# Kernel optimization log

Hardware: AMD Instinct MI355X
Metric: run time of the kernel (lower is better)

The kernel has to match this reference:

```python
import jax, jax.numpy as jnp
import numpy as np

B, K, D = 4096, 16, 256
NUM_CODES = 512
BETA = 0.25  # commitment (activation_entropy=None path)
LN_EPS = 1e-5

def setup_inputs() -> dict:
    key = jax.random.key(0)
    ks = jax.random.split(key, 6)
    hidden = jax.random.normal(ks[0], (B, K, D), dtype=jnp.float32)
    active_mask = jax.random.randint(ks[1], (B, K), 0, 2).astype(bool)
    bound = 1.0 / NUM_CODES
    codebook = jax.random.uniform(ks[2], (NUM_CODES, D), minval=-bound, maxval=bound, dtype=jnp.float32)
    lim = 1.0 / np.sqrt(D)
    W_in = jax.random.uniform(ks[3], (D, D), minval=-lim, maxval=lim, dtype=jnp.float32)
    W_out = jax.random.uniform(ks[4], (D, D), minval=-lim, maxval=lim, dtype=jnp.float32)
    ln_gamma = jnp.ones((D,), jnp.float32)
    ln_beta = jnp.zeros((D,), jnp.float32)
    return {"hidden": hidden, "active_mask": active_mask, "codebook": codebook,
            "W_in": W_in, "W_out": W_out, "ln_gamma": ln_gamma, "ln_beta": ln_beta}

def reference(hidden, active_mask, codebook, W_in, W_out, ln_gamma, ln_beta):
    sg = jax.lax.stop_gradient
    z = jnp.einsum('bkd,ed->bke', hidden, W_in)              # proj_in (no bias)
    z_flat = z.reshape(-1, D)                                 # [B*K, D]
    # ||z - c||^2 = |z|^2 - 2 z.c + |c|^2
    dist = (jnp.sum(z_flat * z_flat, -1, keepdims=True)
            - 2.0 * z_flat @ codebook.T
            + jnp.sum(codebook * codebook, -1))               # [B*K, C]
    idx = jnp.argmin(dist, axis=-1)                           # [B*K]
    z_q = codebook[idx].reshape(z.shape)                      # gather
    vq_loss = jnp.mean((sg(z_q) - z) ** 2) + BETA * jnp.mean((z_q - sg(z)) ** 2)
    z_st = z + sg(z_q - z)                                    # straight-through
    out = jnp.einsum('bkd,ed->bke', z_st, W_out)              # proj_out
    h = hidden + active_mask[..., None].astype(jnp.float32) * out
    mu = jnp.mean(h, -1, keepdims=True)
    var = jnp.mean((h - mu) ** 2, -1, keepdims=True)
    h_comm = (h - mu) * jax.lax.rsqrt(var + LN_EPS) * ln_gamma + ln_beta
    return h_comm, vq_loss
```

## Files before the change

kernel.cpp:

```cpp
#include <hip/hip_runtime.h>

#define LN_EPS 1e-5f

typedef short bf16x8 __attribute__((ext_vector_type(8)));
typedef float f32x4  __attribute__((ext_vector_type(4)));

__device__ __forceinline__ unsigned short f2bf(float f) {
  unsigned u = __float_as_uint(f);
  u += 0x7fffu + ((u >> 16) & 1u);
  return (unsigned short)(u >> 16);
}
__device__ __forceinline__ float bf2f(unsigned short s) {
  return __uint_as_float(((unsigned)s) << 16);
}

__device__ __forceinline__ bf16x8 pack8(float4 a, float4 b) {
  bf16x8 v;
  v[0] = (short)f2bf(a.x); v[1] = (short)f2bf(a.y);
  v[2] = (short)f2bf(a.z); v[3] = (short)f2bf(a.w);
  v[4] = (short)f2bf(b.x); v[5] = (short)f2bf(b.y);
  v[6] = (short)f2bf(b.z); v[7] = (short)f2bf(b.w);
  return v;
}

__global__ __launch_bounds__(256) void prep_kernel(
    const float* __restrict__ codebook, const float* __restrict__ W_in,
    const float* __restrict__ W_out,
    float* __restrict__ loss_acc, unsigned* __restrict__ ticket,
    float* __restrict__ c2, float* __restrict__ code_out,
    unsigned short* __restrict__ BT) {
  const int b = blockIdx.x, t = threadIdx.x;
  __shared__ float As[32][260];
  __shared__ float Bs[16][260];
  __shared__ float Res[32][17];

  if (b < 64) {
    if (b == 0 && t == 0) { *loss_acc = 0.f; *ticket = 0u; }
    int code = b * 8 + (t >> 5);
    const float* src = codebook + (size_t)code * 256 + (t & 31) * 8;
    float4 x0 = *(const float4*)src, x1 = *(const float4*)(src + 4);
    float s = x0.x * x0.x + x0.y * x0.y + x0.z * x0.z + x0.w * x0.w +
              x1.x * x1.x + x1.y * x1.y + x1.z * x1.z + x1.w * x1.w;
    s += __shfl_xor(s, 1);  s += __shfl_xor(s, 2);
    s += __shfl_xor(s, 4);  s += __shfl_xor(s, 8);
    s += __shfl_xor(s, 16);
    if ((t & 31) == 0) c2[code] = s;
    return;
  }

  if (b < 320) {
    int bi = b - 64, ci = bi & 15, ei = bi >> 4;
    {
      int row = t >> 4, col = (t & 15) * 16;
      const float4* s = (const float4*)(W_out + (size_t)(ei * 16 + row) * 256 + col);
      float4* d = (float4*)&Bs[row][col];
      d[0] = s[0]; d[1] = s[1]; d[2] = s[2]; d[3] = s[3];
    }
    {
      int row = t >> 3, col = (t & 7) * 32;
      const float4* s = (const float4*)(codebook + (size_t)(ci * 32 + row) * 256 + col);
      float4* d = (float4*)&As[row][col];
      #pragma unroll
      for (int k = 0; k < 8; k++) d[k] = s[k];
    }
    __syncthreads();
    int c = t & 31, e0 = t >> 5;
    float a0 = 0.f, a1 = 0.f;
    #pragma unroll 4
    for (int d = 0; d < 256; d += 4) {
      float4 cv = *(const float4*)&As[c][d];
      float4 w0 = *(const float4*)&Bs[e0][d];
      float4 w1 = *(const float4*)&Bs[e0 + 8][d];
      a0 += cv.x * w0.x + cv.y * w0.y + cv.z * w0.z + cv.w * w0.w;
      a1 += cv.x * w1.x + cv.y * w1.y + cv.z * w1.z + cv.w * w1.w;
    }
    code_out[(size_t)(ci * 32 + c) * 256 + ei * 16 + e0]     = a0;
    code_out[(size_t)(ci * 32 + c) * 256 + ei * 16 + e0 + 8] = a1;
    return;
  }

  if (b < 576) {
    int bi = b - 320, ci = bi & 15, di = bi >> 4;
    int c0 = ci * 32, d0 = di * 16;
    {
      int e = t;
      const float* src = W_in + (size_t)e * 256 + d0;
      #pragma unroll
      for (int k = 0; k < 4; k++) {
        float4 v = *(const float4*)(src + k * 4);
        Bs[k * 4 + 0][e] = v.x; Bs[k * 4 + 1][e] = v.y;
        Bs[k * 4 + 2][e] = v.z; Bs[k * 4 + 3][e] = v.w;
      }
    }
    {
      int row = t >> 3, col = (t & 7) * 32;
      const float4* s = (const float4*)(codebook + (size_t)(c0 + row) * 256 + col);
      float4* d = (float4*)&As[row][col];
      #pragma unroll
      for (int k = 0; k < 8; k++) d[k] = s[k];
    }
    __syncthreads();
    int c = t & 31, dl = t >> 5;
    float a0 = 0.f, a1 = 0.f;
    #pragma unroll 4
    for (int d = 0; d < 256; d += 4) {
      float4 cv = *(const float4*)&As[c][d];
      float4 w0 = *(const float4*)&Bs[dl][d];
      float4 w1 = *(const float4*)&Bs[dl + 8][d];
      a0 += cv.x * w0.x + cv.y * w0.y + cv.z * w0.z + cv.w * w0.w;
      a1 += cv.x * w1.x + cv.y * w1.y + cv.z * w1.z + cv.w * w1.w;
    }
    Res[c][dl] = a0; Res[c][dl + 8] = a1;
    __syncthreads();
    if (t < 64) {
      int c2i = t & 31, kqo = t >> 5;
      int code = c0 + c2i, dg = d0 + kqo * 8;
      int cl = code & 255;
      int chunk = (code >> 8) * 8 + (dg >> 5);
      int kq = (dg >> 3) & 3;
      float4 x0, x1;
      x0.x = Res[c2i][kqo * 8 + 0]; x0.y = Res[c2i][kqo * 8 + 1];
      x0.z = Res[c2i][kqo * 8 + 2]; x0.w = Res[c2i][kqo * 8 + 3];
      x1.x = Res[c2i][kqo * 8 + 4]; x1.y = Res[c2i][kqo * 8 + 5];
      x1.z = Res[c2i][kqo * 8 + 6]; x1.w = Res[c2i][kqo * 8 + 7];
      *(bf16x8*)(BT + chunk * 8192 + (cl >> 4) * 512 + kq * 128 + (cl & 15) * 8) =
          pack8(x0, x1);
    }
    return;
  }

  {
    int bi = b - 576;
    int ks = bi & 7, bt = bi >> 3;
    int a0c = ks * 32, b0c = bt * 16;
    {
      int e = t;
      const float* srca = W_in + (size_t)e * 256 + a0c;
      #pragma unroll
      for (int k = 0; k < 8; k++) {
        float4 v = *(const float4*)(srca + k * 4);
        As[k * 4 + 0][e] = v.x; As[k * 4 + 1][e] = v.y;
        As[k * 4 + 2][e] = v.z; As[k * 4 + 3][e] = v.w;
      }
      const float* srcb = W_in + (size_t)e * 256 + b0c;
      #pragma unroll
      for (int k = 0; k < 4; k++) {
        float4 v = *(const float4*)(srcb + k * 4);
        Bs[k * 4 + 0][e] = v.x; Bs[k * 4 + 1][e] = v.y;
        Bs[k * 4 + 2][e] = v.z; Bs[k * 4 + 3][e] = v.w;
      }
    }
    __syncthreads();
    int al = t & 31, bl = t >> 5;
    float s0 = 0.f, s1 = 0.f;
    #pragma unroll 4
    for (int d = 0; d < 256; d += 4) {
      float4 av = *(const float4*)&As[al][d];
      float4 w0 = *(const float4*)&Bs[bl][d];
      float4 w1 = *(const float4*)&Bs[bl + 8][d];
      s0 += av.x * w0.x + av.y * w0.y + av.z * w0.z + av.w * w0.w;
      s1 += av.x * w1.x + av.y * w1.y + av.z * w1.z + av.w * w1.w;
    }
    Res[al][bl] = s0; Res[al][bl + 8] = s1;
    __syncthreads();
    if (t < 64) {
      int bcol = t & 15, kqo = t >> 4;
      int cl = b0c + bcol;
      int chunk = 16 + ks;
      float4 x0, x1;
      x0.x = Res[kqo * 8 + 0][bcol]; x0.y = Res[kqo * 8 + 1][bcol];
      x0.z = Res[kqo * 8 + 2][bcol]; x0.w = Res[kqo * 8 + 3][bcol];
      x1.x = Res[kqo * 8 + 4][bcol]; x1.y = Res[kqo * 8 + 5][bcol];
      x1.z = Res[kqo * 8 + 6][bcol]; x1.w = Res[kqo * 8 + 7][bcol];
      *(bf16x8*)(BT + chunk * 8192 + (cl >> 4) * 512 + kqo * 128 + (cl & 15) * 8) =
          pack8(x0, x1);
    }
  }
}

__global__ __launch_bounds__(512, 4) void main_kernel(
    const float* __restrict__ hidden, const int* __restrict__ mask,
    const float* __restrict__ gamma, const float* __restrict__ beta,
    const float* __restrict__ c2g, const float* __restrict__ code_out,
    const unsigned short* __restrict__ BT,
    float* __restrict__ loss_acc, unsigned* __restrict__ ticket,
    float* __restrict__ out) {

  __shared__ unsigned short H[64 * 264];
  __shared__ unsigned sminp[512];
  __shared__ float    lossw[8];
  __shared__ int      ridx[64];

  const int t    = threadIdx.x;
  const int lane = t & 63;
  const int w    = t >> 6;
  const int l15  = lane & 15;
  const int quad = lane >> 4;
  const int row0 = blockIdx.x * 64;

  float ccp[2][2];
  #pragma unroll
  for (int p = 0; p < 2; p++)
    #pragma unroll
    for (int j = 0; j < 2; j++)
      ccp[p][j] = c2g[p * 256 + w * 32 + j * 16 + l15];

  #pragma unroll
  for (int i = 0; i < 4; i++) {
    int flat = (t * 8) + i * 4096;
    int r = flat >> 8, c = flat & 255;
    const float* src = hidden + (size_t)row0 * 256 + flat;
    float4 x0 = *(const float4*)src, x1 = *(const float4*)(src + 4);
    *(bf16x8*)(H + r * 264 + c) = pack8(x0, x1);
  }
  __syncthreads();

  const unsigned short* BTw = BT + w * 1024 + lane * 8;
  const f32x4 zf = {0.f, 0.f, 0.f, 0.f};

  unsigned runp[16];
  #pragma unroll
  for (int r = 0; r < 16; r++) runp[r] = 0xFFFFFFFFu;

  f32x4 acc[4][2];

  #pragma unroll
  for (int pass = 0; pass < 2; pass++) {
    #pragma unroll
    for (int i = 0; i < 4; i++)
      #pragma unroll
      for (int j = 0; j < 2; j++) acc[i][j] = zf;

    #pragma unroll 2
    for (int ks = 0; ks < 8; ks++) {
      const unsigned short* bp = BTw + (pass * 8 + ks) * 8192;
      bf16x8 b0 = *(const bf16x8*)(bp);
      bf16x8 b1 = *(const bf16x8*)(bp + 512);
      bf16x8 a[4];
      #pragma unroll
      for (int i = 0; i < 4; i++)
        a[i] = *(const bf16x8*)(H + (i * 16 + l15) * 264 + ks * 32 + quad * 8);
      #pragma unroll
      for (int i = 0; i < 4; i++) {
        acc[i][0] = __builtin_amdgcn_mfma_f32_16x16x32_bf16(a[i], b0, acc[i][0], 0, 0, 0);
        acc[i][1] = __builtin_amdgcn_mfma_f32_16x16x32_bf16(a[i], b1, acc[i][1], 0, 0, 0);
      }
    }
    #pragma unroll
    for (int i = 0; i < 4; i++)
      #pragma unroll
      for (int j = 0; j < 2; j++) {
        int code = pass * 256 + w * 32 + j * 16 + l15;
        float cc = ccp[pass][j];
        #pragma unroll
        for (int r = 0; r < 4; r++) {
          float m = cc - 2.f * acc[i][j][r];
          unsigned bits = __float_as_uint(m);
          unsigned u = bits ^ (0x80000000u | (unsigned)((int)bits >> 31));
          unsigned p = (u & 0xFFFFFE00u) | (unsigned)code;
          int ri = i * 4 + r;
          runp[ri] = min(runp[ri], p);
        }
      }
  }

  #pragma unroll
  for (int ri = 0; ri < 16; ri++) {
    unsigned v = runp[ri];
    v = min(v, (unsigned)__shfl_xor((int)v, 1));
    v = min(v, (unsigned)__shfl_xor((int)v, 2));
    v = min(v, (unsigned)__shfl_xor((int)v, 4));
    v = min(v, (unsigned)__shfl_xor((int)v, 8));
    if (l15 == 0) {
      int i = ri >> 2, r = ri & 3;
      sminp[w * 64 + (i * 16 + quad * 4 + r)] = v;
    }
  }

  #pragma unroll
  for (int i = 0; i < 4; i++)
    #pragma unroll
    for (int j = 0; j < 2; j++) acc[i][j] = zf;

  #pragma unroll 2
  for (int ks = 0; ks < 8; ks++) {
    const unsigned short* gp = BTw + (16 + ks) * 8192;
    bf16x8 g0 = *(const bf16x8*)(gp);
    bf16x8 g1 = *(const bf16x8*)(gp + 512);
    bf16x8 a[4];
    #pragma unroll
    for (int i = 0; i < 4; i++)
      a[i] = *(const bf16x8*)(H + (i * 16 + l15) * 264 + ks * 32 + quad * 8);
    #pragma unroll
    for (int i = 0; i < 4; i++) {
      acc[i][0] = __builtin_amdgcn_mfma_f32_16x16x32_bf16(g0, a[i], acc[i][0], 0, 0, 0);
      acc[i][1] = __builtin_amdgcn_mfma_f32_16x16x32_bf16(g1, a[i], acc[i][1], 0, 0, 0);
    }
  }
  {
    float lsum = 0.f;
    #pragma unroll
    for (int i = 0; i < 4; i++)
      #pragma unroll
      for (int j = 0; j < 2; j++) {
        const unsigned short* hp =
            H + (i * 16 + l15) * 264 + w * 32 + j * 16 + quad * 4;
        uint2 hv = *(const uint2*)hp;
        lsum += acc[i][j][0] * bf2f((unsigned short)(hv.x & 0xFFFFu));
        lsum += acc[i][j][1] * bf2f((unsigned short)(hv.x >> 16));
        lsum += acc[i][j][2] * bf2f((unsigned short)(hv.y & 0xFFFFu));
        lsum += acc[i][j][3] * bf2f((unsigned short)(hv.y >> 16));
      }
    #pragma unroll
    for (int m = 1; m < 64; m <<= 1) lsum += __shfl_xor(lsum, m);
    if (lane == 0) lossw[w] = lsum;
  }
  __syncthreads();

  if (t < 64) {
    unsigned bv = sminp[t];
    #pragma unroll
    for (int ww = 1; ww < 8; ww++) bv = min(bv, sminp[ww * 64 + t]);
    ridx[t] = (int)(bv & 511u);
    unsigned u = bv & 0xFFFFFE00u;
    unsigned bits = (u & 0x80000000u) ? (u ^ 0x80000000u) : ~u;
    float dist = __uint_as_float(bits);
    #pragma unroll
    for (int m = 1; m < 64; m <<= 1) dist += __shfl_xor(dist, m);
    if (t == 0) {
      float lw = lossw[0] + lossw[1] + lossw[2] + lossw[3] +
                 lossw[4] + lossw[5] + lossw[6] + lossw[7];
      atomicAdd(loss_acc, dist + lw);
      __threadfence();
      unsigned done = atomicAdd(ticket, 1u);
      if (done == gridDim.x - 1) {
        float total = atomicAdd(loss_acc, 0.f);
        out[16777216] = 1.25f * total * (1.f / 16777216.f);
      }
    }
  }
  __syncthreads();

  {
    float4 g4 = *(const float4*)(gamma + lane * 4);
    float4 b4 = *(const float4*)(beta + lane * 4);
    for (int rr = 0; rr < 8; rr++) {
      int row = w * 8 + rr;
      int gr  = row0 + row;
      float4 h = *(const float4*)(hidden + (size_t)gr * 256 + lane * 4);
      int code = ridx[row];
      float4 o = *(const float4*)(code_out + (size_t)code * 256 + lane * 4);
      float mf = mask[gr] ? 1.f : 0.f;
      h.x += mf * o.x; h.y += mf * o.y; h.z += mf * o.z; h.w += mf * o.w;
      float s  = h.x + h.y + h.z + h.w;
      float sq = h.x * h.x + h.y * h.y + h.z * h.z + h.w * h.w;
      #pragma unroll
      for (int m = 1; m < 64; m <<= 1) { s += __shfl_xor(s, m); sq += __shfl_xor(sq, m); }
      float mean = s * (1.f / 256.f);
      float var  = sq * (1.f / 256.f) - mean * mean;
      float rstd = rsqrtf(var + LN_EPS);
      float4 res;
      res.x = (h.x - mean) * rstd * g4.x + b4.x;
      res.y = (h.y - mean) * rstd * g4.y + b4.y;
      res.z = (h.z - mean) * rstd * g4.z + b4.z;
      res.w = (h.w - mean) * rstd * g4.w + b4.w;
      *(float4*)(out + (size_t)gr * 256 + lane * 4) = res;
    }
  }
}

extern "C" void kernel_launch(void* const* d_in, const int* in_sizes, int n_in,
                              void* d_out, int out_size, void* d_ws, size_t ws_size,
                              hipStream_t stream) {
  (void)in_sizes; (void)n_in; (void)out_size; (void)ws_size;
  const float* hidden   = (const float*)d_in[0];
  const int*   mask     = (const int*)d_in[1];
  const float* codebook = (const float*)d_in[2];
  const float* W_in     = (const float*)d_in[3];
  const float* W_out    = (const float*)d_in[4];
  const float* gamma    = (const float*)d_in[5];
  const float* beta     = (const float*)d_in[6];
  float* out = (float*)d_out;

  float* wsf      = (float*)d_ws;
  float* loss_acc = wsf;
  unsigned* ticket = (unsigned*)(wsf + 1);
  float* c2       = wsf + 64;
  float* code_out = wsf + 64 + 512;
  unsigned short* BT = (unsigned short*)(wsf + 64 + 512 + 512 * 256);

  prep_kernel<<<704, 256, 0, stream>>>(codebook, W_in, W_out, loss_acc, ticket,
                                       c2, code_out, BT);
  main_kernel<<<1024, 512, 0, stream>>>(hidden, mask, gamma, beta, c2, code_out,
                                        BT, loss_acc, ticket, out);
}
```

Baseline: 197.2 us.

## Halve main kernel threads with 4x4 MFMA tiles and restructured LayerNorm epilogue

```diff
diff --git a/kernel.cpp b/kernel.cpp
--- a/kernel.cpp
+++ b/kernel.cpp
@@ -30,8 +30,8 @@
     float* __restrict__ c2, float* __restrict__ code_out,
     unsigned short* __restrict__ BT) {
   const int b = blockIdx.x, t = threadIdx.x;
-  __shared__ float As[32][260];
-  __shared__ float Bs[16][260];
+  __shared__ float As[32][268];
+  __shared__ float Bs[16][268];
   __shared__ float Res[32][17];
 
   if (b < 64) {
@@ -178,7 +178,7 @@
   }
 }
 
-__global__ __launch_bounds__(512, 4) void main_kernel(
+__global__ __launch_bounds__(256, 4) void main_kernel(
     const float* __restrict__ hidden, const int* __restrict__ mask,
     const float* __restrict__ gamma, const float* __restrict__ beta,
     const float* __restrict__ c2g, const float* __restrict__ code_out,
@@ -187,8 +187,8 @@
     float* __restrict__ out) {
 
   __shared__ unsigned short H[64 * 264];
-  __shared__ unsigned sminp[512];
-  __shared__ float    lossw[8];
+  __shared__ unsigned sminp[256];
+  __shared__ float    lossw[4];
   __shared__ int      ridx[64];
 
   const int t    = threadIdx.x;
@@ -198,16 +198,9 @@
   const int quad = lane >> 4;
   const int row0 = blockIdx.x * 64;
 
-  float ccp[2][2];
   #pragma unroll
-  for (int p = 0; p < 2; p++)
-    #pragma unroll
-    for (int j = 0; j < 2; j++)
-      ccp[p][j] = c2g[p * 256 + w * 32 + j * 16 + l15];
-
-  #pragma unroll
-  for (int i = 0; i < 4; i++) {
-    int flat = (t * 8) + i * 4096;
+  for (int i = 0; i < 8; i++) {
+    int flat = t * 8 + i * 2048;
     int r = flat >> 8, c = flat & 255;
     const float* src = hidden + (size_t)row0 * 256 + flat;
     float4 x0 = *(const float4*)src, x1 = *(const float4*)(src + 4);
@@ -215,43 +208,43 @@
   }
   __syncthreads();
 
-  const unsigned short* BTw = BT + w * 1024 + lane * 8;
+  const unsigned short* BTw = BT + w * 2048 + lane * 8;
   const f32x4 zf = {0.f, 0.f, 0.f, 0.f};
 
   unsigned runp[16];
   #pragma unroll
   for (int r = 0; r < 16; r++) runp[r] = 0xFFFFFFFFu;
 
-  f32x4 acc[4][2];
+  f32x4 acc[4][4];
 
   #pragma unroll
   for (int pass = 0; pass < 2; pass++) {
     #pragma unroll
     for (int i = 0; i < 4; i++)
       #pragma unroll
-      for (int j = 0; j < 2; j++) acc[i][j] = zf;
+      for (int j = 0; j < 4; j++) acc[i][j] = zf;
 
     #pragma unroll 2
     for (int ks = 0; ks < 8; ks++) {
       const unsigned short* bp = BTw + (pass * 8 + ks) * 8192;
-      bf16x8 b0 = *(const bf16x8*)(bp);
-      bf16x8 b1 = *(const bf16x8*)(bp + 512);
       bf16x8 a[4];
       #pragma unroll
       for (int i = 0; i < 4; i++)
         a[i] = *(const bf16x8*)(H + (i * 16 + l15) * 264 + ks * 32 + quad * 8);
       #pragma unroll
-      for (int i = 0; i < 4; i++) {
-        acc[i][0] = __builtin_amdgcn_mfma_f32_16x16x32_bf16(a[i], b0, acc[i][0], 0, 0, 0);
-        acc[i][1] = __builtin_amdgcn_mfma_f32_16x16x32_bf16(a[i], b1, acc[i][1], 0, 0, 0);
-      }
-    }
-    #pragma unroll
-    for (int i = 0; i < 4; i++)
-      #pragma unroll
-      for (int j = 0; j < 2; j++) {
-        int code = pass * 256 + w * 32 + j * 16 + l15;
-        float cc = ccp[pass][j];
+      for (int j = 0; j < 4; j++) {
+        bf16x8 bj = *(const bf16x8*)(bp + j * 512);
+        #pragma unroll
+        for (int i = 0; i < 4; i++)
+          acc[i][j] = __builtin_amdgcn_mfma_f32_16x16x32_bf16(a[i], bj, acc[i][j], 0, 0, 0);
+      }
+    }
+    #pragma unroll
+    for (int j = 0; j < 4; j++) {
+      int code = pass * 256 + w * 64 + j * 16 + l15;
+      float cc = c2g[code];
+      #pragma unroll
+      for (int i = 0; i < 4; i++)
         #pragma unroll
         for (int r = 0; r < 4; r++) {
           float m = cc - 2.f * acc[i][j][r];
@@ -261,7 +254,7 @@
           int ri = i * 4 + r;
           runp[ri] = min(runp[ri], p);
         }
-      }
+    }
   }
 
   #pragma unroll
@@ -280,21 +273,21 @@
   #pragma unroll
   for (int i = 0; i < 4; i++)
     #pragma unroll
-    for (int j = 0; j < 2; j++) acc[i][j] = zf;
+    for (int j = 0; j < 4; j++) acc[i][j] = zf;
 
   #pragma unroll 2
   for (int ks = 0; ks < 8; ks++) {
     const unsigned short* gp = BTw + (16 + ks) * 8192;
-    bf16x8 g0 = *(const bf16x8*)(gp);
-    bf16x8 g1 = *(const bf16x8*)(gp + 512);
     bf16x8 a[4];
     #pragma unroll
     for (int i = 0; i < 4; i++)
       a[i] = *(const bf16x8*)(H + (i * 16 + l15) * 264 + ks * 32 + quad * 8);
     #pragma unroll
-    for (int i = 0; i < 4; i++) {
-      acc[i][0] = __builtin_amdgcn_mfma_f32_16x16x32_bf16(g0, a[i], acc[i][0], 0, 0, 0);
-      acc[i][1] = __builtin_amdgcn_mfma_f32_16x16x32_bf16(g1, a[i], acc[i][1], 0, 0, 0);
+    for (int j = 0; j < 4; j++) {
+      bf16x8 gj = *(const bf16x8*)(gp + j * 512);
+      #pragma unroll
+      for (int i = 0; i < 4; i++)
+        acc[i][j] = __builtin_amdgcn_mfma_f32_16x16x32_bf16(gj, a[i], acc[i][j], 0, 0, 0);
     }
   }
   {
@@ -302,9 +295,9 @@
     #pragma unroll
     for (int i = 0; i < 4; i++)
       #pragma unroll
-      for (int j = 0; j < 2; j++) {
+      for (int j = 0; j < 4; j++) {
         const unsigned short* hp =
-            H + (i * 16 + l15) * 264 + w * 32 + j * 16 + quad * 4;
+            H + (i * 16 + l15) * 264 + w * 64 + j * 16 + quad * 4;
         uint2 hv = *(const uint2*)hp;
         lsum += acc[i][j][0] * bf2f((unsigned short)(hv.x & 0xFFFFu));
         lsum += acc[i][j][1] * bf2f((unsigned short)(hv.x >> 16));
@@ -317,19 +310,69 @@
   }
   __syncthreads();
 
+  unsigned bv = 0xFFFFFFFFu;
   if (t < 64) {
-    unsigned bv = sminp[t];
-    #pragma unroll
-    for (int ww = 1; ww < 8; ww++) bv = min(bv, sminp[ww * 64 + t]);
+    bv = sminp[t];
+    #pragma unroll
+    for (int ww = 1; ww < 4; ww++) bv = min(bv, sminp[ww * 64 + t]);
     ridx[t] = (int)(bv & 511u);
+  }
+  __syncthreads();
+
+  {
+    const int rowg = lane >> 3;
+    const int part = lane & 7;
+    #pragma unroll
+    for (int rr = 0; rr < 2; rr++) {
+      int row = w * 16 + rr * 8 + rowg;
+      int gr  = row0 + row;
+      float mf = mask[gr] ? 1.f : 0.f;
+      int code = ridx[row];
+      const float* hsrc = hidden   + (size_t)gr * 256 + part * 32;
+      const float* osrc = code_out + (size_t)code * 256 + part * 32;
+      float s = 0.f, sq = 0.f;
+      #pragma unroll
+      for (int k = 0; k < 8; k++) {
+        float4 h4 = *(const float4*)(hsrc + k * 4);
+        float4 o4 = *(const float4*)(osrc + k * 4);
+        float a0 = h4.x + mf * o4.x, a1 = h4.y + mf * o4.y;
+        float a2 = h4.z + mf * o4.z, a3 = h4.w + mf * o4.w;
+        s  += (a0 + a1) + (a2 + a3);
+        sq += (a0 * a0 + a1 * a1) + (a2 * a2 + a3 * a3);
+      }
+      s += __shfl_xor(s, 1);  sq += __shfl_xor(sq, 1);
+      s += __shfl_xor(s, 2);  sq += __shfl_xor(sq, 2);
+      s += __shfl_xor(s, 4);  sq += __shfl_xor(sq, 4);
+      float mean = s * (1.f / 256.f);
+      float var  = sq * (1.f / 256.f) - mean * mean;
+      float rstd = rsqrtf(var + LN_EPS);
+      float* dst = out + (size_t)gr * 256 + part * 32;
+      const float* gsrc = gamma + part * 32;
+      const float* bsrc = beta  + part * 32;
+      #pragma unroll
+      for (int k = 0; k < 8; k++) {
+        float4 h4 = *(const float4*)(hsrc + k * 4);
+        float4 o4 = *(const float4*)(osrc + k * 4);
+        float4 g4 = *(const float4*)(gsrc + k * 4);
+        float4 b4 = *(const float4*)(bsrc + k * 4);
+        float4 res;
+        res.x = (h4.x + mf * o4.x - mean) * rstd * g4.x + b4.x;
+        res.y = (h4.y + mf * o4.y - mean) * rstd * g4.y + b4.y;
+        res.z = (h4.z + mf * o4.z - mean) * rstd * g4.z + b4.z;
+        res.w = (h4.w + mf * o4.w - mean) * rstd * g4.w + b4.w;
+        *(float4*)(dst + k * 4) = res;
+      }
+    }
+  }
+
+  if (t < 64) {
     unsigned u = bv & 0xFFFFFE00u;
     unsigned bits = (u & 0x80000000u) ? (u ^ 0x80000000u) : ~u;
     float dist = __uint_as_float(bits);
     #pragma unroll
     for (int m = 1; m < 64; m <<= 1) dist += __shfl_xor(dist, m);
     if (t == 0) {
-      float lw = lossw[0] + lossw[1] + lossw[2] + lossw[3] +
-                 lossw[4] + lossw[5] + lossw[6] + lossw[7];
+      float lw = lossw[0] + lossw[1] + lossw[2] + lossw[3];
       atomicAdd(loss_acc, dist + lw);
       __threadfence();
       unsigned done = atomicAdd(ticket, 1u);
@@ -337,34 +380,6 @@
         float total = atomicAdd(loss_acc, 0.f);
         out[16777216] = 1.25f * total * (1.f / 16777216.f);
       }
-    }
-  }
-  __syncthreads();
-
-  {
-    float4 g4 = *(const float4*)(gamma + lane * 4);
-    float4 b4 = *(const float4*)(beta + lane * 4);
-    for (int rr = 0; rr < 8; rr++) {
-      int row = w * 8 + rr;
-      int gr  = row0 + row;
-      float4 h = *(const float4*)(hidden + (size_t)gr * 256 + lane * 4);
-      int code = ridx[row];
-      float4 o = *(const float4*)(code_out + (size_t)code * 256 + lane * 4);
-      float mf = mask[gr] ? 1.f : 0.f;
-      h.x += mf * o.x; h.y += mf * o.y; h.z += mf * o.z; h.w += mf * o.w;
-      float s  = h.x + h.y + h.z + h.w;
-      float sq = h.x * h.x + h.y * h.y + h.z * h.z + h.w * h.w;
-      #pragma unroll
-      for (int m = 1; m < 64; m <<= 1) { s += __shfl_xor(s, m); sq += __shfl_xor(sq, m); }
-      float mean = s * (1.f / 256.f);
-      float var  = sq * (1.f / 256.f) - mean * mean;
-      float rstd = rsqrtf(var + LN_EPS);
-      float4 res;
-      res.x = (h.x - mean) * rstd * g4.x + b4.x;
-      res.y = (h.y - mean) * rstd * g4.y + b4.y;
-      res.z = (h.z - mean) * rstd * g4.z + b4.z;
-      res.w = (h.w - mean) * rstd * g4.w + b4.w;
-      *(float4*)(out + (size_t)gr * 256 + lane * 4) = res;
     }
   }
 }
@@ -391,6 +406,6 @@
 
   prep_kernel<<<704, 256, 0, stream>>>(codebook, W_in, W_out, loss_acc, ticket,
                                        c2, code_out, BT);
-  main_kernel<<<1024, 512, 0, stream>>>(hidden, mask, gamma, beta, c2, code_out,
+  main_kernel<<<1024, 256, 0, stream>>>(hidden, mask, gamma, beta, c2, code_out,
                                         BT, loss_acc, ticket, out);
 }
```

New measurement: 356.0 us. 80.5% more time.
